# Performance work log

Measured on AMD Instinct MI355X. Metric: run time of the kernel, lower is better.

The kernel has to match this reference:

```python
import jax, jax.numpy as jnp
import numpy as np

N_NODES = 50000
N_EDGES = 1600000
D = 128


def setup_inputs() -> dict:
    key = jax.random.key(0)
    ks = jax.random.split(key, 8)
    features = jax.random.normal(ks[0], (N_NODES, D), dtype=jnp.float32)
    edge_src = jax.random.randint(ks[1], (N_EDGES,), 0, N_NODES, dtype=jnp.int32)
    edge_dst = jax.random.randint(ks[2], (N_EDGES,), 0, N_NODES, dtype=jnp.int32)
    edge_weight = jax.random.uniform(ks[3], (N_EDGES,), dtype=jnp.float32)
    scale = 1.0 / np.sqrt(D)
    W1 = jax.random.normal(ks[4], (D, D), dtype=jnp.float32) * scale
    b1 = jnp.zeros((D,), dtype=jnp.float32)
    W2 = jax.random.normal(ks[5], (D, D), dtype=jnp.float32) * scale
    b2 = jnp.zeros((D,), dtype=jnp.float32)
    return {"features": features, "edge_src": edge_src, "edge_dst": edge_dst,
            "edge_weight": edge_weight, "W1": W1, "b1": b1, "W2": W2, "b2": b2}


def _gcn_layer(x, W, b, edge_src, edge_dst, edge_weight, n_nodes):
    # support = X @ W  (dense projection), then spmm: out[d] += w_e * support[s]
    support = x @ W  # [N, D]
    msgs = support[edge_src] * edge_weight[:, None]  # [E, D] gather + scale
    out = jax.ops.segment_sum(msgs, edge_dst, num_segments=n_nodes)  # scatter-add
    return out + b


def reference(features, edge_src, edge_dst, edge_weight, W1, b1, W2, b2):
    h = _gcn_layer(features, W1, b1, edge_src, edge_dst, edge_weight, N_NODES)
    h = jax.nn.relu(h)
    # dropout is identity in eval mode (training=False)
    out = _gcn_layer(h, W2, b2, edge_src, edge_dst, edge_weight, N_NODES)
    return out
```

## Files before the change

kernel.cpp:

```cpp
#include <hip/hip_runtime.h>
#include <hip/hip_fp16.h>
#include <math.h>

#define D 128
#define BSHIFT 7
#define BSIZE (1 << BSHIFT)
#define CHUNK 4096
#define BT 1024
#define CAP 7168
#define BSTR 16
#define LDP 136
#define SENTV 0xFFFFFFFFu

typedef _Float16 half8 __attribute__((ext_vector_type(8)));
typedef float f32x4 __attribute__((ext_vector_type(4)));
typedef float f32x2 __attribute__((ext_vector_type(2)));

#if __has_builtin(__builtin_amdgcn_cvt_pk_f32_fp8) && \
    __has_builtin(__builtin_amdgcn_cvt_pk_fp8_f32)
#define HAVE_FP8_CVT 1
#endif

__device__ __forceinline__ float dec_e4m3(unsigned int b) {
    const unsigned int e = (b >> 3) & 0xF;
    const unsigned int m = b & 7;
    float v;
    if (e == 0) v = (float)m * 0.001953125f;
    else        v = (float)(8 + m) * __uint_as_float((e + 117) << 23);
    return (b & 0x80) ? -v : v;
}

__device__ __forceinline__ unsigned char enc_fp8(float x) {
#ifdef HAVE_FP8_CVT
    return (unsigned char)(__builtin_amdgcn_cvt_pk_fp8_f32(x, x, 0, false) & 0xFF);
#else
    const float ax0 = fabsf(x);
    const unsigned int s = (x < 0.f) ? 0x80u : 0u;
    const float ax = fminf(ax0, 448.0f);
    if (ax < 0.015625f) {
        const int m = __float2int_rn(ax * 512.0f);
        return (unsigned char)(s | (unsigned int)m);
    }
    int ex;
    const float fr = frexpf(ax, &ex);
    int m = __float2int_rn(fr * 16.0f) - 8;
    int e = ex - 1 + 7;
    if (m == 8) { m = 0; e += 1; }
    if (e > 15) return (unsigned char)(s | 0x7E);
    return (unsigned char)(s | ((unsigned int)e << 3) | (unsigned int)m);
#endif
}

__global__ __launch_bounds__(512) void init_bcur(int* __restrict__ bcur, int NB) {
    const int b = blockIdx.x * 512 + threadIdx.x;
    if (b < NB) bcur[b * BSTR] = b * CAP;
}

__device__ __forceinline__ void gemm_body_f32(const float* __restrict__ X,
                                              const __half* __restrict__ Wt,
                                              unsigned char* __restrict__ Y,
                                              int M, int bx) {
    const int lane = threadIdx.x & 63;
    const int wv = threadIdx.x >> 6;
    const int row0 = bx * 256 + wv * 16;
    const int m = lane & 15;
    const int q = lane >> 4;

    if (row0 >= M) return;
    const int rsafe = min(row0 + m, M - 1);
    const float4* Xr = (const float4*)(X + (size_t)rsafe * D);
    half8 a[4];
#pragma unroll
    for (int kt = 0; kt < 4; ++kt) {
        const float4 lo = Xr[kt * 8 + q * 2];
        const float4 hi = Xr[kt * 8 + q * 2 + 1];
        a[kt] = (half8){(_Float16)lo.x, (_Float16)lo.y, (_Float16)lo.z,
                        (_Float16)lo.w, (_Float16)hi.x, (_Float16)hi.y,
                        (_Float16)hi.z, (_Float16)hi.w};
    }

    const half8* WT8 = (const half8*)Wt;
#pragma unroll
    for (int ct = 0; ct < 8; ++ct) {
        const int n = ct * 16 + m;
        f32x4 acc = {0.f, 0.f, 0.f, 0.f};
#pragma unroll
        for (int kt = 0; kt < 4; ++kt) {
            const half8 b = WT8[(size_t)n * 16 + kt * 4 + q];
            acc = __builtin_amdgcn_mfma_f32_16x16x32_f16(a[kt], b, acc, 0, 0, 0);
        }
#pragma unroll
        for (int r = 0; r < 4; ++r) {
            const int orow = row0 + q * 4 + r;
            if (orow < M)
                Y[(size_t)orow * D + ct * 16 + m] = enc_fp8(acc[r]);
        }
    }
}

__global__ __launch_bounds__(BT) void scatter_prep(const int* __restrict__ src,
                                                   const int* __restrict__ dst,
                                                   const float* __restrict__ wgt,
                                                   int* __restrict__ bcur,
                                                   unsigned int* __restrict__ csrA,
                                                   int E, int NB, int nscat,
                                                   const float* __restrict__ W1,
                                                   const float* __restrict__ W2,
                                                   __half* __restrict__ W1t,
                                                   __half* __restrict__ W2t) {
    if (blockIdx.x >= (unsigned)nscat) {
        const int which = blockIdx.x - nscat;
        const float* W = which ? W2 : W1;
        __half* Wt = which ? W2t : W1t;
        for (int i = threadIdx.x; i < D * D; i += BT) {
            const int n = i >> 7, k = i & 127;
            Wt[i] = __float2half(W[k * D + n]);
        }
        return;
    }

    __shared__ int lhist[512];
    __shared__ int lstart[512];
    __shared__ int lcur[512];
    const int tid = threadIdx.x;
    const int base = blockIdx.x * CHUNK;

    for (int b = tid; b < NB; b += BT) lhist[b] = 0;
    __syncthreads();

    int dreg[CHUNK / BT];
#pragma unroll
    for (int u = 0; u < CHUNK / BT; ++u) {
        const int e = base + u * BT + tid;
        dreg[u] = (e < E) ? dst[e] : -1;
        if (dreg[u] >= 0) atomicAdd(&lhist[dreg[u] >> BSHIFT], 1);
    }
    __syncthreads();

    for (int b = tid; b < NB; b += BT) {
        const int c = lhist[b];
        if (c) {
            const int r = atomicAdd(&bcur[b * BSTR], (c + 15) & ~15);
            lstart[b] = r;
            lcur[b] = r;
        }
    }
    __syncthreads();

#pragma unroll
    for (int u = 0; u < CHUNK / BT; ++u) {
        const int d = dreg[u];
        if (d >= 0) {
            const int e = base + u * BT + tid;
            const int b = d >> BSHIFT;
            const int pos = atomicAdd(&lcur[b], 1);
            const unsigned int wq =
                (unsigned int)__float2int_rn(wgt[e] * 511.0f);
            const unsigned int kv = (unsigned int)src[e] |
                                    ((unsigned int)(d & (BSIZE - 1)) << 16) |
                                    (wq << 23);
            if (pos < (b + 1) * CAP) csrA[pos] = kv;
        }
    }
    __syncthreads();

    for (int b = tid; b < NB; b += BT) {
        const int c = lhist[b];
        if (c) {
            const int beg = lstart[b] + c;
            const int fin = lstart[b] + ((c + 15) & ~15);
            for (int p = beg; p < fin; ++p)
                if (p < (b + 1) * CAP) csrA[p] = SENTV;
        }
    }
}

__global__ __launch_bounds__(BT) void sort_gemm1(const unsigned int* __restrict__ csrA,
                                                 const int* __restrict__ bcur,
                                                 int* __restrict__ offsets,
                                                 int* __restrict__ deg,
                                                 unsigned int* __restrict__ csr,
                                                 int M, int NB,
                                                 const float* __restrict__ X,
                                                 const __half* __restrict__ W1t,
                                                 unsigned char* __restrict__ sup) {
    if (blockIdx.x >= (unsigned)NB) {
        gemm_body_f32(X, W1t, sup, M, blockIdx.x - NB);
        return;
    }

    __shared__ int hist[BSIZE];
    __shared__ int ncur[BSIZE];
    __shared__ int wtot[2];
    const int b = blockIdx.x;
    const int n0 = b << BSHIFT;
    const int tid = threadIdx.x;
    const int nloc = min(BSIZE, M - n0);
    const int bstart = b * CAP;
    const int bend = min(bcur[b * BSTR], (b + 1) * CAP);

    if (tid < BSIZE) hist[tid] = 0;
    __syncthreads();

    unsigned int reg[CAP / BT];
#pragma unroll
    for (int i = 0; i < CAP / BT; ++i) {
        const int j = bstart + i * BT + tid;
        unsigned int kv = SENTV;
        if (j < bend) kv = csrA[j];
        reg[i] = kv;
        if ((kv & 0xFFFFu) != 0xFFFFu)
            atomicAdd(&hist[(kv >> 16) & (BSIZE - 1)], 1);
    }
    __syncthreads();

    const int lane = tid & 63;
    const int wv = tid >> 6;
    const int v = (tid < BSIZE) ? hist[tid] : 0;
    int incl = v;
#pragma unroll
    for (int off = 1; off < 64; off <<= 1) {
        int t = __shfl_up(incl, off, 64);
        if (lane >= off) incl += t;
    }
    if (tid < BSIZE && lane == 63) wtot[wv] = incl;
    __syncthreads();
    const int carry = (wv == 1) ? wtot[0] : 0;
    const int excl = bstart + incl - v + carry;
    if (tid < nloc) {
        offsets[n0 + tid] = excl;
        deg[n0 + tid] = v;
        ncur[tid] = excl;
    }
    __syncthreads();

#pragma unroll
    for (int i = 0; i < CAP / BT; ++i) {
        const unsigned int kv = reg[i];
        if ((kv & 0xFFFFu) != 0xFFFFu) {
            const int pos = atomicAdd(&ncur[(kv >> 16) & (BSIZE - 1)], 1);
            csr[pos] = kv;
        }
    }
}

__device__ __forceinline__ void accum8(float acc[8], uint2 raw, float w) {
#ifdef HAVE_FP8_CVT
    const f32x2 f01 = __builtin_amdgcn_cvt_pk_f32_fp8(raw.x, false);
    const f32x2 f23 = __builtin_amdgcn_cvt_pk_f32_fp8(raw.x, true);
    const f32x2 f45 = __builtin_amdgcn_cvt_pk_f32_fp8(raw.y, false);
    const f32x2 f67 = __builtin_amdgcn_cvt_pk_f32_fp8(raw.y, true);
    acc[0] = fmaf(w, f01[0], acc[0]);
    acc[1] = fmaf(w, f01[1], acc[1]);
    acc[2] = fmaf(w, f23[0], acc[2]);
    acc[3] = fmaf(w, f23[1], acc[3]);
    acc[4] = fmaf(w, f45[0], acc[4]);
    acc[5] = fmaf(w, f45[1], acc[5]);
    acc[6] = fmaf(w, f67[0], acc[6]);
    acc[7] = fmaf(w, f67[1], acc[7]);
#else
#pragma unroll
    for (int i = 0; i < 4; ++i)
        acc[i] = fmaf(w, dec_e4m3((raw.x >> (8 * i)) & 0xFF), acc[i]);
#pragma unroll
    for (int i = 0; i < 4; ++i)
        acc[4 + i] = fmaf(w, dec_e4m3((raw.y >> (8 * i)) & 0xFF), acc[4 + i]);
#endif
}

__device__ __forceinline__ float kv_w(unsigned int kv) {
    return (float)(kv >> 23) * (1.0f / 511.0f);
}

__device__ __forceinline__ void gather_row(const uint2* __restrict__ supv,
                                           const unsigned int* __restrict__ csr,
                                           int beg, int end, int l, float acc[8]) {
    int j = beg;
    for (; j + 16 <= end; j += 16) {
        unsigned int kv[16];
        uint2 r[16];
#pragma unroll
        for (int u = 0; u < 16; ++u) kv[u] = csr[j + u];
#pragma unroll
        for (int u = 0; u < 16; ++u)
            r[u] = supv[(size_t)(kv[u] & 0xFFFF) * 16 + l];
#pragma unroll
        for (int u = 0; u < 16; ++u) accum8(acc, r[u], kv_w(kv[u]));
    }
    if (j + 8 <= end) {
        unsigned int kv[8];
        uint2 r[8];
#pragma unroll
        for (int u = 0; u < 8; ++u) kv[u] = csr[j + u];
#pragma unroll
        for (int u = 0; u < 8; ++u)
            r[u] = supv[(size_t)(kv[u] & 0xFFFF) * 16 + l];
#pragma unroll
        for (int u = 0; u < 8; ++u) accum8(acc, r[u], kv_w(kv[u]));
        j += 8;
    }
    if (j + 4 <= end) {
        unsigned int kv[4];
        uint2 r[4];
#pragma unroll
        for (int u = 0; u < 4; ++u) kv[u] = csr[j + u];
#pragma unroll
        for (int u = 0; u < 4; ++u)
            r[u] = supv[(size_t)(kv[u] & 0xFFFF) * 16 + l];
#pragma unroll
        for (int u = 0; u < 4; ++u) accum8(acc, r[u], kv_w(kv[u]));
        j += 4;
    }
    for (; j < end; ++j) {
        const unsigned int kv = csr[j];
        const uint2 r = supv[(size_t)(kv & 0xFFFF) * 16 + l];
        accum8(acc, r, kv_w(kv));
    }
}

__global__ __launch_bounds__(256) void gather_gemm(const unsigned char* __restrict__ sup,
                                                   const int* __restrict__ offsets,
                                                   const int* __restrict__ deg,
                                                   const unsigned int* __restrict__ csr,
                                                   const float* __restrict__ b1,
                                                   const __half* __restrict__ W2t,
                                                   unsigned char* __restrict__ sup2,
                                                   int M) {
    __shared__ _Float16 hA[16 * LDP];
    const int tid = threadIdx.x;
    const int q = tid >> 4;
    const int l = tid & 15;
    const int n = blockIdx.x * 16 + q;

    float acc[8];
    {
        const float4 c0 = ((const float4*)b1)[l * 2];
        const float4 c1 = ((const float4*)b1)[l * 2 + 1];
        acc[0] = c0.x; acc[1] = c0.y; acc[2] = c0.z; acc[3] = c0.w;
        acc[4] = c1.x; acc[5] = c1.y; acc[6] = c1.z; acc[7] = c1.w;
    }
    if (n < M) {
        const int beg = offsets[n];
        gather_row((const uint2*)sup, csr, beg, beg + deg[n], l, acc);
    }

    half8 hv;
#pragma unroll
    for (int i = 0; i < 8; ++i) hv[i] = (_Float16)fmaxf(acc[i], 0.f);
    *(half8*)&hA[q * LDP + l * 8] = hv;
    __syncthreads();

    const int lane = tid & 63;
    const int wv = tid >> 6;
    const int m = lane & 15;
    const int qq = lane >> 4;
    half8 a[4];
#pragma unroll
    for (int kt = 0; kt < 4; ++kt)
        a[kt] = *(const half8*)&hA[m * LDP + kt * 32 + qq * 8];

    const half8* WT8 = (const half8*)W2t;
#pragma unroll
    for (int c = 0; c < 2; ++c) {
        const int ct = wv * 2 + c;
        const int ncol = ct * 16 + m;
        f32x4 dacc = {0.f, 0.f, 0.f, 0.f};
#pragma unroll
        for (int kt = 0; kt < 4; ++kt) {
            const half8 b = WT8[(size_t)ncol * 16 + kt * 4 + qq];
            dacc = __builtin_amdgcn_mfma_f32_16x16x32_f16(a[kt], b, dacc, 0, 0, 0);
        }
#pragma unroll
        for (int r = 0; r < 4; ++r) {
            const int orow = blockIdx.x * 16 + qq * 4 + r;
            if (orow < M)
                sup2[(size_t)orow * D + ct * 16 + m] = enc_fp8(dacc[r]);
        }
    }
}

__global__ __launch_bounds__(256) void gather_out(const unsigned char* __restrict__ sup,
                                                  const int* __restrict__ offsets,
                                                  const int* __restrict__ deg,
                                                  const unsigned int* __restrict__ csr,
                                                  const float* __restrict__ bias,
                                                  float* __restrict__ out, int M) {
    const int tid = threadIdx.x;
    const int q = tid >> 4;
    const int l = tid & 15;
    const int n = blockIdx.x * 16 + q;
    if (n >= M) return;

    float acc[8];
    {
        const float4 c0 = ((const float4*)bias)[l * 2];
        const float4 c1 = ((const float4*)bias)[l * 2 + 1];
        acc[0] = c0.x; acc[1] = c0.y; acc[2] = c0.z; acc[3] = c0.w;
        acc[4] = c1.x; acc[5] = c1.y; acc[6] = c1.z; acc[7] = c1.w;
    }
    const int beg = offsets[n];
    gather_row((const uint2*)sup, csr, beg, beg + deg[n], l, acc);

    f32x4* out4 = (f32x4*)out;
    const f32x4 o0 = {acc[0], acc[1], acc[2], acc[3]};
    const f32x4 o1 = {acc[4], acc[5], acc[6], acc[7]};
    __builtin_nontemporal_store(o0, out4 + (size_t)n * 32 + l * 2);
    __builtin_nontemporal_store(o1, out4 + (size_t)n * 32 + l * 2 + 1);
}

extern "C" void kernel_launch(void* const* d_in, const int* in_sizes, int n_in,
                              void* d_out, int out_size, void* d_ws, size_t ws_size,
                              hipStream_t stream) {
    const float* features = (const float*)d_in[0];
    const int*   esrc     = (const int*)d_in[1];
    const int*   edst     = (const int*)d_in[2];
    const float* ew       = (const float*)d_in[3];
    const float* W1       = (const float*)d_in[4];
    const float* b1       = (const float*)d_in[5];
    const float* W2       = (const float*)d_in[6];
    const float* b2       = (const float*)d_in[7];
    float* out = (float*)d_out;

    const int M = in_sizes[0] / D;
    const int E = in_sizes[1];
    const int NB = (M + BSIZE - 1) >> BSHIFT;

    unsigned int* csrA = (unsigned int*)d_ws;
    unsigned int* csr  = csrA + (size_t)NB * CAP;
    unsigned char* sup = (unsigned char*)(csr + (size_t)NB * CAP);
    unsigned char* sup2 = sup + (size_t)M * D;
    int*    offsets = (int*)(sup2 + (size_t)M * D);
    int*    deg     = offsets + M;
    int*    bcur    = deg + M;
    __half* W1t     = (__half*)(bcur + (size_t)NB * BSTR);
    __half* W2t     = W1t + D * D;

    const int gemm_blocks = (M + 255) / 256;
    const int node_blocks = (M + 15) / 16;
    const int nscat = (E + CHUNK - 1) / CHUNK;

    init_bcur<<<1, 512, 0, stream>>>(bcur, NB);
    scatter_prep<<<nscat + 2, BT, 0, stream>>>(esrc, edst, ew, bcur, csrA, E, NB,
                                               nscat, W1, W2, W1t, W2t);
    sort_gemm1<<<NB + gemm_blocks, BT, 0, stream>>>(csrA, bcur, offsets, deg, csr,
                                                    M, NB, features, W1t, sup);
    gather_gemm<<<node_blocks, 256, 0, stream>>>(sup, offsets, deg, csr, b1, W2t,
                                                 sup2, M);
    gather_out<<<node_blocks, 256, 0, stream>>>(sup2, offsets, deg, csr, b2, out, M);
}
```

Baseline: 211.4 us.

## Fuse bucket sort into layer-one gather and move GEMM1 alongside edge scatter

```diff
diff --git a/kernel.cpp b/kernel.cpp
--- a/kernel.cpp
+++ b/kernel.cpp
@@ -9,7 +9,7 @@
 #define BT 1024
 #define CAP 7168
 #define BSTR 16
-#define LDP 136
+#define LDP 132
 #define SENTV 0xFFFFFFFFu
 
 typedef _Float16 half8 __attribute__((ext_vector_type(8)));
@@ -51,9 +51,23 @@
 #endif
 }
 
-__global__ __launch_bounds__(512) void init_bcur(int* __restrict__ bcur, int NB) {
-    const int b = blockIdx.x * 512 + threadIdx.x;
-    if (b < NB) bcur[b * BSTR] = b * CAP;
+__global__ __launch_bounds__(512) void init_misc(int* __restrict__ bcur, int NB,
+                                                 const float* __restrict__ W1,
+                                                 const float* __restrict__ W2,
+                                                 __half* __restrict__ W1t,
+                                                 __half* __restrict__ W2t) {
+    if (blockIdx.x == 0) {
+        const int b = threadIdx.x;
+        if (b < NB) bcur[b * BSTR] = b * CAP;
+        return;
+    }
+    const int which = blockIdx.x - 1;
+    const float* W = which ? W2 : W1;
+    __half* Wt = which ? W2t : W1t;
+    for (int i = threadIdx.x; i < D * D; i += 512) {
+        const int n = i >> 7, k = i & 127;
+        Wt[i] = __float2half(W[k * D + n]);
+    }
 }
 
 __device__ __forceinline__ void gemm_body_f32(const float* __restrict__ X,
@@ -98,32 +112,25 @@
     }
 }
 
-__global__ __launch_bounds__(BT) void scatter_prep(const int* __restrict__ src,
-                                                   const int* __restrict__ dst,
-                                                   const float* __restrict__ wgt,
-                                                   int* __restrict__ bcur,
-                                                   unsigned int* __restrict__ csrA,
-                                                   int E, int NB, int nscat,
-                                                   const float* __restrict__ W1,
-                                                   const float* __restrict__ W2,
-                                                   __half* __restrict__ W1t,
-                                                   __half* __restrict__ W2t) {
-    if (blockIdx.x >= (unsigned)nscat) {
-        const int which = blockIdx.x - nscat;
-        const float* W = which ? W2 : W1;
-        __half* Wt = which ? W2t : W1t;
-        for (int i = threadIdx.x; i < D * D; i += BT) {
-            const int n = i >> 7, k = i & 127;
-            Wt[i] = __float2half(W[k * D + n]);
-        }
+__global__ __launch_bounds__(BT) void scatter_gemm1(const int* __restrict__ src,
+                                                    const int* __restrict__ dst,
+                                                    const float* __restrict__ wgt,
+                                                    int* __restrict__ bcur,
+                                                    unsigned int* __restrict__ csrA,
+                                                    int E, int NB, int gemmb,
+                                                    const float* __restrict__ X,
+                                                    const __half* __restrict__ W1t,
+                                                    unsigned char* __restrict__ sup,
+                                                    int M) {
+    if (blockIdx.x < (unsigned)gemmb) {
+        gemm_body_f32(X, W1t, sup, M, blockIdx.x);
         return;
     }
-
     __shared__ int lhist[512];
     __shared__ int lstart[512];
     __shared__ int lcur[512];
     const int tid = threadIdx.x;
-    const int base = blockIdx.x * CHUNK;
+    const int base = (blockIdx.x - gemmb) * CHUNK;
 
     for (int b = tid; b < NB; b += BT) lhist[b] = 0;
     __syncthreads();
@@ -171,75 +178,6 @@
             const int fin = lstart[b] + ((c + 15) & ~15);
             for (int p = beg; p < fin; ++p)
                 if (p < (b + 1) * CAP) csrA[p] = SENTV;
-        }
-    }
-}
-
-__global__ __launch_bounds__(BT) void sort_gemm1(const unsigned int* __restrict__ csrA,
-                                                 const int* __restrict__ bcur,
-                                                 int* __restrict__ offsets,
-                                                 int* __restrict__ deg,
-                                                 unsigned int* __restrict__ csr,
-                                                 int M, int NB,
-                                                 const float* __restrict__ X,
-                                                 const __half* __restrict__ W1t,
-                                                 unsigned char* __restrict__ sup) {
-    if (blockIdx.x >= (unsigned)NB) {
-        gemm_body_f32(X, W1t, sup, M, blockIdx.x - NB);
-        return;
-    }
-
-    __shared__ int hist[BSIZE];
-    __shared__ int ncur[BSIZE];
-    __shared__ int wtot[2];
-    const int b = blockIdx.x;
-    const int n0 = b << BSHIFT;
-    const int tid = threadIdx.x;
-    const int nloc = min(BSIZE, M - n0);
-    const int bstart = b * CAP;
-    const int bend = min(bcur[b * BSTR], (b + 1) * CAP);
-
-    if (tid < BSIZE) hist[tid] = 0;
-    __syncthreads();
-
-    unsigned int reg[CAP / BT];
-#pragma unroll
-    for (int i = 0; i < CAP / BT; ++i) {
-        const int j = bstart + i * BT + tid;
-        unsigned int kv = SENTV;
-        if (j < bend) kv = csrA[j];
-        reg[i] = kv;
-        if ((kv & 0xFFFFu) != 0xFFFFu)
-            atomicAdd(&hist[(kv >> 16) & (BSIZE - 1)], 1);
-    }
-    __syncthreads();
-
-    const int lane = tid & 63;
-    const int wv = tid >> 6;
-    const int v = (tid < BSIZE) ? hist[tid] : 0;
-    int incl = v;
-#pragma unroll
-    for (int off = 1; off < 64; off <<= 1) {
-        int t = __shfl_up(incl, off, 64);
-        if (lane >= off) incl += t;
-    }
-    if (tid < BSIZE && lane == 63) wtot[wv] = incl;
-    __syncthreads();
-    const int carry = (wv == 1) ? wtot[0] : 0;
-    const int excl = bstart + incl - v + carry;
-    if (tid < nloc) {
-        offsets[n0 + tid] = excl;
-        deg[n0 + tid] = v;
-        ncur[tid] = excl;
-    }
-    __syncthreads();
-
-#pragma unroll
-    for (int i = 0; i < CAP / BT; ++i) {
-        const unsigned int kv = reg[i];
-        if ((kv & 0xFFFFu) != 0xFFFFu) {
-            const int pos = atomicAdd(&ncur[(kv >> 16) & (BSIZE - 1)], 1);
-            csr[pos] = kv;
         }
     }
 }
@@ -318,61 +256,169 @@
     }
 }
 
-__global__ __launch_bounds__(256) void gather_gemm(const unsigned char* __restrict__ sup,
-                                                   const int* __restrict__ offsets,
-                                                   const int* __restrict__ deg,
-                                                   const unsigned int* __restrict__ csr,
-                                                   const float* __restrict__ b1,
-                                                   const __half* __restrict__ W2t,
-                                                   unsigned char* __restrict__ sup2,
-                                                   int M) {
-    __shared__ _Float16 hA[16 * LDP];
+__device__ __forceinline__ void gather_row_lds(const uint2* __restrict__ supv,
+                                               const unsigned int* ekv2,
+                                               int beg, int end, int l, float acc[8]) {
+    int j = beg;
+    for (; j + 16 <= end; j += 16) {
+        unsigned int kv[16];
+        uint2 r[16];
+#pragma unroll
+        for (int u = 0; u < 16; ++u) kv[u] = ekv2[j + u];
+#pragma unroll
+        for (int u = 0; u < 16; ++u)
+            r[u] = supv[(size_t)(kv[u] & 0xFFFF) * 16 + l];
+#pragma unroll
+        for (int u = 0; u < 16; ++u) accum8(acc, r[u], kv_w(kv[u]));
+    }
+    if (j + 8 <= end) {
+        unsigned int kv[8];
+        uint2 r[8];
+#pragma unroll
+        for (int u = 0; u < 8; ++u) kv[u] = ekv2[j + u];
+#pragma unroll
+        for (int u = 0; u < 8; ++u)
+            r[u] = supv[(size_t)(kv[u] & 0xFFFF) * 16 + l];
+#pragma unroll
+        for (int u = 0; u < 8; ++u) accum8(acc, r[u], kv_w(kv[u]));
+        j += 8;
+    }
+    if (j + 4 <= end) {
+        unsigned int kv[4];
+        uint2 r[4];
+#pragma unroll
+        for (int u = 0; u < 4; ++u) kv[u] = ekv2[j + u];
+#pragma unroll
+        for (int u = 0; u < 4; ++u)
+            r[u] = supv[(size_t)(kv[u] & 0xFFFF) * 16 + l];
+#pragma unroll
+        for (int u = 0; u < 4; ++u) accum8(acc, r[u], kv_w(kv[u]));
+        j += 4;
+    }
+    for (; j < end; ++j) {
+        const unsigned int kv = ekv2[j];
+        const uint2 r = supv[(size_t)(kv & 0xFFFF) * 16 + l];
+        accum8(acc, r, kv_w(kv));
+    }
+}
+
+__global__ __launch_bounds__(BT) void gather_sort_gemm(
+    const unsigned int* __restrict__ csrA, const int* __restrict__ bcur,
+    int* __restrict__ offsets, int* __restrict__ deg,
+    unsigned int* __restrict__ csr,
+    const unsigned char* __restrict__ sup, const float* __restrict__ b1,
+    const __half* __restrict__ W2t, unsigned char* __restrict__ sup2, int M) {
+    __shared__ unsigned int ekv2[CAP];
+    __shared__ _Float16 hA[BSIZE * LDP];
+    __shared__ int hist[BSIZE];
+    __shared__ int loff[BSIZE];
+    __shared__ int ldeg[BSIZE];
+    __shared__ int ncur[BSIZE];
+    __shared__ int wtot[2];
+
+    const int b = blockIdx.x;
+    const int n0 = b << BSHIFT;
     const int tid = threadIdx.x;
-    const int q = tid >> 4;
+    const int nloc = min(BSIZE, M - n0);
+    const int bstart = b * CAP;
+    const int bend = min(bcur[b * BSTR], bstart + CAP);
+
+    if (tid < BSIZE) hist[tid] = 0;
+    __syncthreads();
+
+    unsigned int reg[CAP / BT];
+#pragma unroll
+    for (int i = 0; i < CAP / BT; ++i) {
+        const int j = bstart + i * BT + tid;
+        unsigned int kv = SENTV;
+        if (j < bend) kv = csrA[j];
+        reg[i] = kv;
+        if ((kv & 0xFFFFu) != 0xFFFFu)
+            atomicAdd(&hist[(kv >> 16) & (BSIZE - 1)], 1);
+    }
+    __syncthreads();
+
+    const int lane = tid & 63;
+    const int wv = tid >> 6;
+    const int v = (tid < BSIZE) ? hist[tid] : 0;
+    int incl = v;
+#pragma unroll
+    for (int off = 1; off < 64; off <<= 1) {
+        int t = __shfl_up(incl, off, 64);
+        if (lane >= off) incl += t;
+    }
+    if (tid < BSIZE && lane == 63) wtot[wv] = incl;
+    __syncthreads();
+    if (tid < BSIZE) {
+        const int carry = (wv == 1) ? wtot[0] : 0;
+        const int ex = incl - v + carry;
+        loff[tid] = ex;
+        ldeg[tid] = v;
+        ncur[tid] = ex;
+        if (tid < nloc) {
+            offsets[n0 + tid] = bstart + ex;
+            deg[n0 + tid] = v;
+        }
+    }
+    for (int i = tid; i < (BSIZE - nloc) * LDP; i += BT)
+        hA[nloc * LDP + i] = (_Float16)0.f;
+    __syncthreads();
+
+#pragma unroll
+    for (int i = 0; i < CAP / BT; ++i) {
+        const unsigned int kv = reg[i];
+        if ((kv & 0xFFFFu) != 0xFFFFu) {
+            const int pos = atomicAdd(&ncur[(kv >> 16) & (BSIZE - 1)], 1);
+            ekv2[pos] = kv;
+        }
+    }
+    __syncthreads();
+
+#pragma unroll
+    for (int i = 0; i < CAP / BT; ++i)
+        csr[bstart + i * BT + tid] = ekv2[i * BT + tid];
+
+    const int grp = tid >> 4;
     const int l = tid & 15;
-    const int n = blockIdx.x * 16 + q;
-
-    float acc[8];
-    {
-        const float4 c0 = ((const float4*)b1)[l * 2];
-        const float4 c1 = ((const float4*)b1)[l * 2 + 1];
+    const uint2* supv = (const uint2*)sup;
+    const float4 c0 = ((const float4*)b1)[l * 2];
+    const float4 c1 = ((const float4*)b1)[l * 2 + 1];
+    for (int n = grp; n < nloc; n += 64) {
+        float acc[8];
         acc[0] = c0.x; acc[1] = c0.y; acc[2] = c0.z; acc[3] = c0.w;
         acc[4] = c1.x; acc[5] = c1.y; acc[6] = c1.z; acc[7] = c1.w;
-    }
-    if (n < M) {
-        const int beg = offsets[n];
-        gather_row((const uint2*)sup, csr, beg, beg + deg[n], l, acc);
-    }
-
-    half8 hv;
-#pragma unroll
-    for (int i = 0; i < 8; ++i) hv[i] = (_Float16)fmaxf(acc[i], 0.f);
-    *(half8*)&hA[q * LDP + l * 8] = hv;
-    __syncthreads();
-
-    const int lane = tid & 63;
-    const int wv = tid >> 6;
+        const int beg = loff[n];
+        gather_row_lds(supv, ekv2, beg, beg + ldeg[n], l, acc);
+        half8 hv;
+#pragma unroll
+        for (int i = 0; i < 8; ++i) hv[i] = (_Float16)fmaxf(acc[i], 0.f);
+        *(half8*)&hA[n * LDP + l * 8] = hv;
+    }
+    __syncthreads();
+
     const int m = lane & 15;
     const int qq = lane >> 4;
+    const int rt = wv >> 1;
+    const int ct0 = (wv & 1) * 4;
     half8 a[4];
 #pragma unroll
     for (int kt = 0; kt < 4; ++kt)
-        a[kt] = *(const half8*)&hA[m * LDP + kt * 32 + qq * 8];
+        a[kt] = *(const half8*)&hA[(rt * 16 + m) * LDP + kt * 32 + qq * 8];
 
     const half8* WT8 = (const half8*)W2t;
 #pragma unroll
-    for (int c = 0; c < 2; ++c) {
-        const int ct = wv * 2 + c;
+    for (int c = 0; c < 4; ++c) {
+        const int ct = ct0 + c;
         const int ncol = ct * 16 + m;
         f32x4 dacc = {0.f, 0.f, 0.f, 0.f};
 #pragma unroll
         for (int kt = 0; kt < 4; ++kt) {
-            const half8 b = WT8[(size_t)ncol * 16 + kt * 4 + qq];
-            dacc = __builtin_amdgcn_mfma_f32_16x16x32_f16(a[kt], b, dacc, 0, 0, 0);
+            const half8 bb = WT8[(size_t)ncol * 16 + kt * 4 + qq];
+            dacc = __builtin_amdgcn_mfma_f32_16x16x32_f16(a[kt], bb, dacc, 0, 0, 0);
         }
 #pragma unroll
         for (int r = 0; r < 4; ++r) {
-            const int orow = blockIdx.x * 16 + qq * 4 + r;
+            const int orow = n0 + rt * 16 + qq * 4 + r;
             if (orow < M)
                 sup2[(size_t)orow * D + ct * 16 + m] = enc_fp8(dacc[r]);
         }
@@ -435,16 +481,14 @@
     __half* W1t     = (__half*)(bcur + (size_t)NB * BSTR);
     __half* W2t     = W1t + D * D;
 
-    const int gemm_blocks = (M + 255) / 256;
+    const int gemmb = (M + 255) / 256;
     const int node_blocks = (M + 15) / 16;
     const int nscat = (E + CHUNK - 1) / CHUNK;
 
-    init_bcur<<<1, 512, 0, stream>>>(bcur, NB);
-    scatter_prep<<<nscat + 2, BT, 0, stream>>>(esrc, edst, ew, bcur, csrA, E, NB,
-                                               nscat, W1, W2, W1t, W2t);
-    sort_gemm1<<<NB + gemm_blocks, BT, 0, stream>>>(csrA, bcur, offsets, deg, csr,
-                                                    M, NB, features, W1t, sup);
-    gather_gemm<<<node_blocks, 256, 0, stream>>>(sup, offsets, deg, csr, b1, W2t,
-                                                 sup2, M);
+    init_misc<<<3, 512, 0, stream>>>(bcur, NB, W1, W2, W1t, W2t);
+    scatter_gemm1<<<gemmb + nscat, BT, 0, stream>>>(esrc, edst, ew, bcur, csrA, E,
+                                                    NB, gemmb, features, W1t, sup, M);
+    gather_sort_gemm<<<NB, BT, 0, stream>>>(csrA, bcur, offsets, deg, csr, sup, b1,
+                                            W2t, sup2, M);
     gather_out<<<node_blocks, 256, 0, stream>>>(sup2, offsets, deg, csr, b2, out, M);
 }
```

After: 223.0 us. 5.5% more time.
